# Kernel optimization log

Hardware: AMD Instinct MI355X
Metric: run time of the kernel (lower is better)

## Reference

```python
import jax, jax.numpy as jnp
import numpy as np

B, D, R, E, L = 16384, 1024, 64, 4, 3  # batch, in_features, low_rank, expert_num, layer_num


def setup_inputs() -> dict:
    key = jax.random.key(0)
    k0, k1, k2, k3, k4 = jax.random.split(key, 5)
    x = jax.random.normal(k0, (B, D), dtype=jnp.float32)
    # xavier_normal-ish init scales
    su = (2.0 / (D + R)) ** 0.5
    sc = (2.0 / (R + R)) ** 0.5
    U = jax.random.normal(k1, (L, E, D, R), dtype=jnp.float32) * su
    V = jax.random.normal(k2, (L, E, R, D), dtype=jnp.float32) * su
    C = jax.random.normal(k3, (L, E, R, R), dtype=jnp.float32) * sc
    bias = jnp.zeros((L, D), dtype=jnp.float32)  # original (L, D, 1) squeezed
    gates_w = jax.random.normal(k4, (E, D), dtype=jnp.float32) * (1.0 / D ** 0.5)
    return {"x": x, "U": U, "V": V, "C": C, "bias": bias, "gates_w": gates_w}


def reference(x, U, V, C, bias, gates_w):
    x0 = x                                  # [B, D]
    xl = x
    n_layers = U.shape[0]
    for i in range(n_layers):               # small fixed layer count
        g = jax.nn.softmax(xl @ gates_w.T, axis=1)          # [B, E] softmax over experts
        t = jnp.tanh(jnp.einsum('erd,bd->ber', V[i], xl))   # [B, E, R]
        t = jnp.tanh(jnp.einsum('ers,bes->ber', C[i], t))   # [B, E, R]
        t = jnp.einsum('edr,ber->bed', U[i], t) + bias[i][None, None, :]  # [B, E, D]
        t = x0[:, None, :] * t                               # x0 * E_i(xl)
        xl = jnp.einsum('bed,be->bd', t, g) + xl             # gated combine + residual
    return xl
```

## Files before the change

### kernel.cpp

```cpp
#include <hip/hip_runtime.h>
#include <hip/hip_bf16.h>


using bf16x8 = __attribute__((ext_vector_type(8))) short;
using f32x4  = __attribute__((ext_vector_type(4))) float;

__device__ __forceinline__ unsigned short f2bf(float f) {
  union { __hip_bfloat16 h; unsigned short s; } u;
  u.h = __float2bfloat16(f);
  return u.s;
}
__device__ __forceinline__ float fast_tanh(float x) {
  float cx = fminf(15.0f, fmaxf(-15.0f, x));
  float t = exp2f(cx * 2.885390081777927f);
  return (t - 1.0f) / (t + 1.0f);
}

__global__ void preconvert_k(const float4* __restrict__ V4, const float4* __restrict__ U4,
                             const float4* __restrict__ C4, const float4* __restrict__ G4,
                             ushort4* __restrict__ Vb4, ushort4* __restrict__ Ub4,
                             ushort4* __restrict__ Cb4, ushort4* __restrict__ Gb4) {
  int i = blockIdx.x * 256 + threadIdx.x;
  if (i < 196608) {
    float4 v = V4[i], u = U4[i];
    ushort4 ov, ou;
    ov.x = f2bf(v.x); ov.y = f2bf(v.y); ov.z = f2bf(v.z); ov.w = f2bf(v.w);
    ou.x = f2bf(u.x); ou.y = f2bf(u.y); ou.z = f2bf(u.z); ou.w = f2bf(u.w);
    Vb4[i] = ov; Ub4[i] = ou;
  }
  if (i < 12288) {
    float4 c = C4[i];
    ushort4 oc; oc.x = f2bf(c.x); oc.y = f2bf(c.y); oc.z = f2bf(c.z); oc.w = f2bf(c.w);
    Cb4[i] = oc;
  }
  if (i < 1024) {
    float4 g = G4[i];
    ushort4 og; og.x = f2bf(g.x); og.y = f2bf(g.y); og.z = f2bf(g.z); og.w = f2bf(g.w);
    Gb4[i] = og;
  }
}

__global__ __launch_bounds__(1024, 4)
void crossmix_fused(const float* __restrict__ x, float* __restrict__ out,
                    const unsigned short* __restrict__ Vb,
                    const unsigned short* __restrict__ Ub,
                    const unsigned short* __restrict__ Cb,
                    const unsigned short* __restrict__ Gb,
                    const float* __restrict__ bias) {
  constexpr int BM = 32, DD = 1024;
  __shared__ unsigned short xl_lds[BM * DD];
  __shared__ unsigned short tbuf[BM * 256];
  __shared__ float g_lds[BM][4];

  const int tid  = threadIdx.x;
  const int lane = tid & 63;
  const int wc   = tid >> 6;
  const int l15  = lane & 15;
  const int l4   = lane >> 4;
  const size_t rowbase = (size_t)blockIdx.x * BM;

  f32x4 zf = {0.f, 0.f, 0.f, 0.f};

  f32x4 xlr[2][4];

  #pragma unroll
  for (int mt = 0; mt < 2; ++mt)
    #pragma unroll
    for (int nt = 0; nt < 4; ++nt)
      #pragma unroll
      for (int rg = 0; rg < 4; ++rg) {
        int rowl = mt * 16 + l4 * 4 + rg;
        int d = wc * 64 + nt * 16 + l15;
        float v = x[(rowbase + rowl) * DD + d];
        xlr[mt][nt][rg] = v;
        *(unsigned short*)((char*)xl_lds + ((rowl * 2048 + d * 2) ^ ((rowl & 7) << 4))) = f2bf(v);
      }
  __syncthreads();

  for (int l = 0; l < 3; ++l) {
    const unsigned short* Vl = Vb + l * 262144;
    const unsigned short* Ul = Ub + l * 262144;
    const unsigned short* Cl = Cb + l * 16384;
    const float* bl = bias + l * 1024;

    f32x4 acc1[2], accg[2];
    acc1[0] = zf; acc1[1] = zf; accg[0] = zf; accg[1] = zf;
    const int ncol = wc * 16;
    #pragma unroll 4
    for (int ks = 0; ks < 32; ++ks) {
      bf16x8 afr[2];
      #pragma unroll
      for (int mt = 0; mt < 2; ++mt) {
        int row = mt * 16 + l15;
        afr[mt] = *(const bf16x8*)((const char*)xl_lds +
                    ((row * 2048 + ks * 64 + l4 * 16) ^ ((row & 7) << 4)));
      }
      int kg = ks * 32 + l4 * 8;
      bf16x8 bfr = *(const bf16x8*)(Vl + (ncol + l15) * 1024 + kg);
      acc1[0] = __builtin_amdgcn_mfma_f32_16x16x32_bf16(afr[0], bfr, acc1[0], 0, 0, 0);
      acc1[1] = __builtin_amdgcn_mfma_f32_16x16x32_bf16(afr[1], bfr, acc1[1], 0, 0, 0);
      if (wc == 0) {
        bf16x8 gfr = {0, 0, 0, 0, 0, 0, 0, 0};
        if (l15 < 4) gfr = *(const bf16x8*)(Gb + l15 * 1024 + kg);
        accg[0] = __builtin_amdgcn_mfma_f32_16x16x32_bf16(afr[0], gfr, accg[0], 0, 0, 0);
        accg[1] = __builtin_amdgcn_mfma_f32_16x16x32_bf16(afr[1], gfr, accg[1], 0, 0, 0);
      }
    }
    #pragma unroll
    for (int mt = 0; mt < 2; ++mt)
      #pragma unroll
      for (int rg = 0; rg < 4; ++rg) {
        int row = mt * 16 + l4 * 4 + rg;
        int col = ncol + l15;
        *(unsigned short*)((char*)tbuf + ((row * 512 + col * 2) ^ ((row & 7) << 4)))
            = f2bf(fast_tanh(acc1[mt][rg]));
      }
    if (wc == 0 && l15 < 4) {
      #pragma unroll
      for (int mt = 0; mt < 2; ++mt)
        #pragma unroll
        for (int rg = 0; rg < 4; ++rg)
          g_lds[mt * 16 + l4 * 4 + rg][l15] = accg[mt][rg];
    }
    __syncthreads();

    if (tid < BM) {
      float a0 = g_lds[tid][0], a1 = g_lds[tid][1], a2 = g_lds[tid][2], a3 = g_lds[tid][3];
      float mx = fmaxf(fmaxf(a0, a1), fmaxf(a2, a3));
      float e0 = exp2f((a0 - mx) * 1.442695041f);
      float e1 = exp2f((a1 - mx) * 1.442695041f);
      float e2 = exp2f((a2 - mx) * 1.442695041f);
      float e3 = exp2f((a3 - mx) * 1.442695041f);
      float inv = 1.0f / (e0 + e1 + e2 + e3);
      g_lds[tid][0] = e0 * inv; g_lds[tid][1] = e1 * inv;
      g_lds[tid][2] = e2 * inv; g_lds[tid][3] = e3 * inv;
    }

    const int ex = wc >> 2, q = wc & 3;
    f32x4 acc2[2];
    acc2[0] = zf; acc2[1] = zf;
    #pragma unroll
    for (int ks = 0; ks < 2; ++ks) {
      bf16x8 afr[2];
      #pragma unroll
      for (int mt = 0; mt < 2; ++mt) {
        int row = mt * 16 + l15;
        afr[mt] = *(const bf16x8*)((const char*)tbuf +
                    ((row * 512 + (ex * 64 + ks * 32 + l4 * 8) * 2) ^ ((row & 7) << 4)));
      }
      bf16x8 bfr = *(const bf16x8*)(Cl + ex * 4096 + (q * 16 + l15) * 64 + ks * 32 + l4 * 8);
      acc2[0] = __builtin_amdgcn_mfma_f32_16x16x32_bf16(afr[0], bfr, acc2[0], 0, 0, 0);
      acc2[1] = __builtin_amdgcn_mfma_f32_16x16x32_bf16(afr[1], bfr, acc2[1], 0, 0, 0);
    }
    __syncthreads();
    #pragma unroll
    for (int mt = 0; mt < 2; ++mt)
      #pragma unroll
      for (int rg = 0; rg < 4; ++rg) {
        int row = mt * 16 + l4 * 4 + rg;
        int col = ex * 64 + q * 16 + l15;
        float gv = g_lds[row][ex];
        *(unsigned short*)((char*)tbuf + ((row * 512 + col * 2) ^ ((row & 7) << 4)))
            = f2bf(gv * fast_tanh(acc2[mt][rg]));
      }
    __syncthreads();

    f32x4 acc3[2][4];
    #pragma unroll
    for (int mt = 0; mt < 2; ++mt)
      #pragma unroll
      for (int nt = 0; nt < 4; ++nt) acc3[mt][nt] = zf;
    #pragma unroll 2
    for (int ks = 0; ks < 8; ++ks) {
      bf16x8 afr[2];
      #pragma unroll
      for (int mt = 0; mt < 2; ++mt) {
        int row = mt * 16 + l15;
        afr[mt] = *(const bf16x8*)((const char*)tbuf +
                    ((row * 512 + (ks * 32 + l4 * 8) * 2) ^ ((row & 7) << 4)));
      }
      int k = ks * 32 + l4 * 8;
      int ee = k >> 6, rr = k & 63;
      #pragma unroll
      for (int nt = 0; nt < 4; ++nt) {
        int d = wc * 64 + nt * 16 + l15;
        bf16x8 bfr = *(const bf16x8*)(Ul + ee * 65536 + d * 64 + rr);
        acc3[0][nt] = __builtin_amdgcn_mfma_f32_16x16x32_bf16(afr[0], bfr, acc3[0][nt], 0, 0, 0);
        acc3[1][nt] = __builtin_amdgcn_mfma_f32_16x16x32_bf16(afr[1], bfr, acc3[1][nt], 0, 0, 0);
      }
    }

    #pragma unroll
    for (int nt = 0; nt < 4; ++nt) {
      int d = wc * 64 + nt * 16 + l15;
      float bv = bl[d];
      #pragma unroll
      for (int mt = 0; mt < 2; ++mt)
        #pragma unroll
        for (int rg = 0; rg < 4; ++rg) {
          int rowl = mt * 16 + l4 * 4 + rg;
          float x0v = x[(rowbase + rowl) * DD + d];
          xlr[mt][nt][rg] += x0v * (bv + acc3[mt][nt][rg]);
        }
    }

    if (l < 2) {
      #pragma unroll
      for (int mt = 0; mt < 2; ++mt)
        #pragma unroll
        for (int nt = 0; nt < 4; ++nt)
          #pragma unroll
          for (int rg = 0; rg < 4; ++rg) {
            int rowl = mt * 16 + l4 * 4 + rg;
            int d = wc * 64 + nt * 16 + l15;
            *(unsigned short*)((char*)xl_lds + ((rowl * 2048 + d * 2) ^ ((rowl & 7) << 4)))
                = f2bf(xlr[mt][nt][rg]);
          }
    }
    __syncthreads();
  }

  #pragma unroll
  for (int mt = 0; mt < 2; ++mt)
    #pragma unroll
    for (int nt = 0; nt < 4; ++nt)
      #pragma unroll
      for (int rg = 0; rg < 4; ++rg) {
        int rowl = mt * 16 + l4 * 4 + rg;
        int d = wc * 64 + nt * 16 + l15;
        out[(rowbase + rowl) * DD + d] = xlr[mt][nt][rg];
      }
}

extern "C" void kernel_launch(void* const* d_in, const int* in_sizes, int n_in,
                              void* d_out, int out_size, void* d_ws, size_t ws_size,
                              hipStream_t stream) {
  const float* x    = (const float*)d_in[0];
  const float* U    = (const float*)d_in[1];
  const float* V    = (const float*)d_in[2];
  const float* C    = (const float*)d_in[3];
  const float* bias = (const float*)d_in[4];
  const float* gw   = (const float*)d_in[5];
  float* out = (float*)d_out;

  unsigned short* Vb = (unsigned short*)d_ws;
  unsigned short* Ub = Vb + 786432;
  unsigned short* Cb = Ub + 786432;
  unsigned short* Gb = Cb + 49152;

  preconvert_k<<<dim3(768), dim3(256), 0, stream>>>(
      (const float4*)V, (const float4*)U, (const float4*)C, (const float4*)gw,
      (ushort4*)Vb, (ushort4*)Ub, (ushort4*)Cb, (ushort4*)Gb);

  crossmix_fused<<<dim3(512), dim3(1024), 0, stream>>>(
      x, out, Vb, Ub, Cb, Gb, bias);
}
```

Before: 461.4 us.

## Halve block to 512 threads with doubled per-wave column work

```diff
diff --git a/kernel.cpp b/kernel.cpp
--- a/kernel.cpp
+++ b/kernel.cpp
@@ -40,7 +40,7 @@
   }
 }
 
-__global__ __launch_bounds__(1024, 4)
+__global__ __launch_bounds__(512, 2)
 void crossmix_fused(const float* __restrict__ x, float* __restrict__ out,
                     const unsigned short* __restrict__ Vb,
                     const unsigned short* __restrict__ Ub,
@@ -61,16 +61,16 @@
 
   f32x4 zf = {0.f, 0.f, 0.f, 0.f};
 
-  f32x4 xlr[2][4];
+  f32x4 xlr[2][8];
 
   #pragma unroll
   for (int mt = 0; mt < 2; ++mt)
     #pragma unroll
-    for (int nt = 0; nt < 4; ++nt)
+    for (int nt = 0; nt < 8; ++nt)
       #pragma unroll
       for (int rg = 0; rg < 4; ++rg) {
         int rowl = mt * 16 + l4 * 4 + rg;
-        int d = wc * 64 + nt * 16 + l15;
+        int d = wc * 128 + nt * 16 + l15;
         float v = x[(rowbase + rowl) * DD + d];
         xlr[mt][nt][rg] = v;
         *(unsigned short*)((char*)xl_lds + ((rowl * 2048 + d * 2) ^ ((rowl & 7) << 4))) = f2bf(v);
@@ -83,9 +83,10 @@
     const unsigned short* Cl = Cb + l * 16384;
     const float* bl = bias + l * 1024;
 
-    f32x4 acc1[2], accg[2];
-    acc1[0] = zf; acc1[1] = zf; accg[0] = zf; accg[1] = zf;
-    const int ncol = wc * 16;
+    f32x4 acc1[2][2], accg[2];
+    #pragma unroll
+    for (int mt = 0; mt < 2; ++mt) { acc1[mt][0] = zf; acc1[mt][1] = zf; accg[mt] = zf; }
+    const int ncol = wc * 32;
     #pragma unroll 4
     for (int ks = 0; ks < 32; ++ks) {
       bf16x8 afr[2];
@@ -96,9 +97,12 @@
                     ((row * 2048 + ks * 64 + l4 * 16) ^ ((row & 7) << 4)));
       }
       int kg = ks * 32 + l4 * 8;
-      bf16x8 bfr = *(const bf16x8*)(Vl + (ncol + l15) * 1024 + kg);
-      acc1[0] = __builtin_amdgcn_mfma_f32_16x16x32_bf16(afr[0], bfr, acc1[0], 0, 0, 0);
-      acc1[1] = __builtin_amdgcn_mfma_f32_16x16x32_bf16(afr[1], bfr, acc1[1], 0, 0, 0);
+      #pragma unroll
+      for (int nt = 0; nt < 2; ++nt) {
+        bf16x8 bfr = *(const bf16x8*)(Vl + (ncol + nt * 16 + l15) * 1024 + kg);
+        acc1[0][nt] = __builtin_amdgcn_mfma_f32_16x16x32_bf16(afr[0], bfr, acc1[0][nt], 0, 0, 0);
+        acc1[1][nt] = __builtin_amdgcn_mfma_f32_16x16x32_bf16(afr[1], bfr, acc1[1][nt], 0, 0, 0);
+      }
       if (wc == 0) {
         bf16x8 gfr = {0, 0, 0, 0, 0, 0, 0, 0};
         if (l15 < 4) gfr = *(const bf16x8*)(Gb + l15 * 1024 + kg);
@@ -109,12 +113,14 @@
     #pragma unroll
     for (int mt = 0; mt < 2; ++mt)
       #pragma unroll
-      for (int rg = 0; rg < 4; ++rg) {
-        int row = mt * 16 + l4 * 4 + rg;
-        int col = ncol + l15;
-        *(unsigned short*)((char*)tbuf + ((row * 512 + col * 2) ^ ((row & 7) << 4)))
-            = f2bf(fast_tanh(acc1[mt][rg]));
-      }
+      for (int nt = 0; nt < 2; ++nt)
+        #pragma unroll
+        for (int rg = 0; rg < 4; ++rg) {
+          int row = mt * 16 + l4 * 4 + rg;
+          int col = ncol + nt * 16 + l15;
+          *(unsigned short*)((char*)tbuf + ((row * 512 + col * 2) ^ ((row & 7) << 4)))
+              = f2bf(fast_tanh(acc1[mt][nt][rg]));
+        }
     if (wc == 0 && l15 < 4) {
       #pragma unroll
       for (int mt = 0; mt < 2; ++mt)
@@ -136,9 +142,10 @@
       g_lds[tid][2] = e2 * inv; g_lds[tid][3] = e3 * inv;
     }
 
-    const int ex = wc >> 2, q = wc & 3;
-    f32x4 acc2[2];
-    acc2[0] = zf; acc2[1] = zf;
+    const int ex = wc >> 1, q = wc & 1;
+    f32x4 acc2[2][2];
+    #pragma unroll
+    for (int mt = 0; mt < 2; ++mt) { acc2[mt][0] = zf; acc2[mt][1] = zf; }
     #pragma unroll
     for (int ks = 0; ks < 2; ++ks) {
       bf16x8 afr[2];
@@ -148,28 +155,33 @@
         afr[mt] = *(const bf16x8*)((const char*)tbuf +
                     ((row * 512 + (ex * 64 + ks * 32 + l4 * 8) * 2) ^ ((row & 7) << 4)));
       }
-      bf16x8 bfr = *(const bf16x8*)(Cl + ex * 4096 + (q * 16 + l15) * 64 + ks * 32 + l4 * 8);
-      acc2[0] = __builtin_amdgcn_mfma_f32_16x16x32_bf16(afr[0], bfr, acc2[0], 0, 0, 0);
-      acc2[1] = __builtin_amdgcn_mfma_f32_16x16x32_bf16(afr[1], bfr, acc2[1], 0, 0, 0);
+      #pragma unroll
+      for (int nt = 0; nt < 2; ++nt) {
+        bf16x8 bfr = *(const bf16x8*)(Cl + ex * 4096 + (q * 32 + nt * 16 + l15) * 64 + ks * 32 + l4 * 8);
+        acc2[0][nt] = __builtin_amdgcn_mfma_f32_16x16x32_bf16(afr[0], bfr, acc2[0][nt], 0, 0, 0);
+        acc2[1][nt] = __builtin_amdgcn_mfma_f32_16x16x32_bf16(afr[1], bfr, acc2[1][nt], 0, 0, 0);
+      }
     }
     __syncthreads();
     #pragma unroll
     for (int mt = 0; mt < 2; ++mt)
       #pragma unroll
-      for (int rg = 0; rg < 4; ++rg) {
-        int row = mt * 16 + l4 * 4 + rg;
-        int col = ex * 64 + q * 16 + l15;
-        float gv = g_lds[row][ex];
-        *(unsigned short*)((char*)tbuf + ((row * 512 + col * 2) ^ ((row & 7) << 4)))
-            = f2bf(gv * fast_tanh(acc2[mt][rg]));
-      }
-    __syncthreads();
-
-    f32x4 acc3[2][4];
+      for (int nt = 0; nt < 2; ++nt)
+        #pragma unroll
+        for (int rg = 0; rg < 4; ++rg) {
+          int row = mt * 16 + l4 * 4 + rg;
+          int col = ex * 64 + q * 32 + nt * 16 + l15;
+          float gv = g_lds[row][ex];
+          *(unsigned short*)((char*)tbuf + ((row * 512 + col * 2) ^ ((row & 7) << 4)))
+              = f2bf(gv * fast_tanh(acc2[mt][nt][rg]));
+        }
+    __syncthreads();
+
+    f32x4 acc3[2][8];
     #pragma unroll
     for (int mt = 0; mt < 2; ++mt)
       #pragma unroll
-      for (int nt = 0; nt < 4; ++nt) acc3[mt][nt] = zf;
+      for (int nt = 0; nt < 8; ++nt) acc3[mt][nt] = zf;
     #pragma unroll 2
     for (int ks = 0; ks < 8; ++ks) {
       bf16x8 afr[2];
@@ -182,8 +194,8 @@
       int k = ks * 32 + l4 * 8;
       int ee = k >> 6, rr = k & 63;
       #pragma unroll
-      for (int nt = 0; nt < 4; ++nt) {
-        int d = wc * 64 + nt * 16 + l15;
+      for (int nt = 0; nt < 8; ++nt) {
+        int d = wc * 128 + nt * 16 + l15;
         bf16x8 bfr = *(const bf16x8*)(Ul + ee * 65536 + d * 64 + rr);
         acc3[0][nt] = __builtin_amdgcn_mfma_f32_16x16x32_bf16(afr[0], bfr, acc3[0][nt], 0, 0, 0);
         acc3[1][nt] = __builtin_amdgcn_mfma_f32_16x16x32_bf16(afr[1], bfr, acc3[1][nt], 0, 0, 0);
@@ -191,8 +203,8 @@
     }
 
     #pragma unroll
-    for (int nt = 0; nt < 4; ++nt) {
-      int d = wc * 64 + nt * 16 + l15;
+    for (int nt = 0; nt < 8; ++nt) {
+      int d = wc * 128 + nt * 16 + l15;
       float bv = bl[d];
       #pragma unroll
       for (int mt = 0; mt < 2; ++mt)
@@ -208,11 +220,11 @@
       #pragma unroll
       for (int mt = 0; mt < 2; ++mt)
         #pragma unroll
-        for (int nt = 0; nt < 4; ++nt)
+        for (int nt = 0; nt < 8; ++nt)
           #pragma unroll
           for (int rg = 0; rg < 4; ++rg) {
             int rowl = mt * 16 + l4 * 4 + rg;
-            int d = wc * 64 + nt * 16 + l15;
+            int d = wc * 128 + nt * 16 + l15;
             *(unsigned short*)((char*)xl_lds + ((rowl * 2048 + d * 2) ^ ((rowl & 7) << 4)))
                 = f2bf(xlr[mt][nt][rg]);
           }
@@ -223,11 +235,11 @@
   #pragma unroll
   for (int mt = 0; mt < 2; ++mt)
     #pragma unroll
-    for (int nt = 0; nt < 4; ++nt)
+    for (int nt = 0; nt < 8; ++nt)
       #pragma unroll
       for (int rg = 0; rg < 4; ++rg) {
         int rowl = mt * 16 + l4 * 4 + rg;
-        int d = wc * 64 + nt * 16 + l15;
+        int d = wc * 128 + nt * 16 + l15;
         out[(rowbase + rowl) * DD + d] = xlr[mt][nt][rg];
       }
 }
@@ -252,6 +264,6 @@
       (const float4*)V, (const float4*)U, (const float4*)C, (const float4*)gw,
       (ushort4*)Vb, (ushort4*)Ub, (ushort4*)Cb, (ushort4*)Gb);
 
-  crossmix_fused<<<dim3(512), dim3(1024), 0, stream>>>(
+  crossmix_fused<<<dim3(512), dim3(512), 0, stream>>>(
       x, out, Vb, Ub, Cb, Gb, bias);
 }
```

Result: slower. 505.5 us (+9.5%).
